# Performance work log

Measured on AMD Instinct MI355X. Metric: run time of the kernel, lower is better.

The kernel has to match this reference:

```python
import jax, jax.numpy as jnp
import numpy as np

N = 50000      # nodes
E = 800000     # edges
D_IN = 128
D_OUT = 128
R = 8          # relation types
EPS = 1e-12    # F.normalize eps


def setup_inputs() -> dict:
    key = jax.random.key(0)
    ks = jax.random.split(key, 10)
    s_in = 1.0 / np.sqrt(D_IN)
    s_out = 1.0 / np.sqrt(D_OUT)
    return {
        "x": jax.random.normal(ks[0], (N, D_IN), jnp.float32),
        "W1": jax.random.normal(ks[1], (R, D_IN, D_OUT), jnp.float32) * s_in,
        "loopW1": jax.random.normal(ks[2], (D_IN, D_OUT), jnp.float32) * s_in,
        "b1": jax.random.normal(ks[3], (D_OUT,), jnp.float32) * 0.01,
        "W2": jax.random.normal(ks[4], (R, D_OUT, D_OUT), jnp.float32) * s_out,
        "loopW2": jax.random.normal(ks[5], (D_OUT, D_OUT), jnp.float32) * s_out,
        "b2": jax.random.normal(ks[6], (D_OUT,), jnp.float32) * 0.01,
        "src": jax.random.randint(ks[7], (E,), 0, N),
        "dst": jax.random.randint(ks[8], (E,), 0, N),
        "etypes": jax.random.randint(ks[9], (E,), 0, R),
    }


def rel_layer(x, src, dst, etypes, W, loopW, b):
    # transform every node by every relation: [R, N, D_out]
    xw = jnp.einsum('ni,rio->rno', x, W)
    # gather per-edge messages: [E, D_out]
    msg = xw[etypes, src]
    # scatter-add to destination nodes
    agg = jax.ops.segment_sum(msg, dst, num_segments=x.shape[0])
    # self-loop + bias (DGL RelGraphConv defaults)
    return agg + x @ loopW + b


def reference(x, W1, loopW1, b1, W2, loopW2, b2, src, dst, etypes):
    h = jax.nn.relu(rel_layer(x, src, dst, etypes, W1, loopW1, b1))
    h = rel_layer(h, src, dst, etypes, W2, loopW2, b2)
    # F.normalize: row-wise L2, eps=1e-12
    nrm = jnp.maximum(jnp.linalg.norm(h, axis=1, keepdims=True), EPS)
    return h / nrm
```

## Files before the change

kernel.cpp:

```cpp
#include <hip/hip_runtime.h>
#include <hip/hip_bf16.h>

#define D 128
#define CH 4096

typedef unsigned int u32;
typedef unsigned short u16;
typedef __attribute__((ext_vector_type(8))) short s16x8;
typedef __attribute__((ext_vector_type(4))) float f32x4;
typedef __attribute__((ext_vector_type(2))) float f32x2;

__device__ __forceinline__ float bf2f(u16 u) {
    union { u32 u; float f; } v; v.u = ((u32)u) << 16; return v.f;
}
__device__ __forceinline__ u16 f2bf(float f) {
    union { float f; u32 u; } v; v.f = f;
    return (u16)((v.u + 0x7fffu + ((v.u >> 16) & 1u)) >> 16);
}
__device__ __forceinline__ u32 pack_bf2(float a, float b) {
    __hip_bfloat162 t = __float22bfloat162_rn(make_float2(a, b));
    union { __hip_bfloat162 t; u32 u; } v; v.t = t; return v.u;
}
__device__ __forceinline__ void unpack2(u32 u, float& lo, float& hi) {
    union { u32 u; float f; } a, b;
    a.u = u << 16; b.u = u & 0xffff0000u;
    lo = a.f; hi = b.f;
}

__global__ void detect_dtype(const u16* __restrict__ x, int* __restrict__ flag) {
    __shared__ int cnt;
    if (threadIdx.x == 0) cnt = 0;
    __syncthreads();
    u16 u = x[2 * threadIdx.x];
    int e = (u >> 7) & 0xFF;
    if (e >= 96 && e <= 150) atomicAdd(&cnt, 1);
    __syncthreads();
    if (threadIdx.x == 0) *flag = (cnt >= 128) ? 0 : 1;
}

__global__ __launch_bounds__(256)
void to_bf16_all(const void* __restrict__ s0, const void* __restrict__ s1,
                 const void* __restrict__ s2, const void* __restrict__ s3,
                 const void* __restrict__ s4, const void* __restrict__ s5,
                 const void* __restrict__ s6,
                 u16* __restrict__ d0, u16* __restrict__ d1, u16* __restrict__ d2,
                 u16* __restrict__ d3, u16* __restrict__ d4, u16* __restrict__ d5,
                 u16* __restrict__ d6,
                 long long n0, long long n1, long long n2, long long n3,
                 long long n4, long long n5, long long n6,
                 const int* __restrict__ flag)
{
    if (*flag == 0) return;
    long long i = (long long)blockIdx.x * 256 + threadIdx.x;
    const void* s; u16* d; long long off;
    if      (i < n0)                   { s = s0; d = d0; off = i; }
    else if (i < n0+n1)                { s = s1; d = d1; off = i-n0; }
    else if (i < n0+n1+n2)             { s = s2; d = d2; off = i-n0-n1; }
    else if (i < n0+n1+n2+n3)          { s = s3; d = d3; off = i-n0-n1-n2; }
    else if (i < n0+n1+n2+n3+n4)       { s = s4; d = d4; off = i-n0-n1-n2-n3; }
    else if (i < n0+n1+n2+n3+n4+n5)    { s = s5; d = d5; off = i-n0-n1-n2-n3-n4; }
    else if (i < n0+n1+n2+n3+n4+n5+n6) { s = s6; d = d6; off = i-n0-n1-n2-n3-n4-n5; }
    else return;
    d[off] = f2bf(((const float*)s)[off]);
}

__global__ __launch_bounds__(256)
void zero_ints(int* __restrict__ a, int n) {
    int i = blockIdx.x * 256 + threadIdx.x;
    if (i < n) a[i] = 0;
}

__global__ __launch_bounds__(256)
void csr_count(const int* __restrict__ dst, int* __restrict__ gcnt, int E, int nbuck) {
    __shared__ int scnt[256];
    int tid = threadIdx.x;
    scnt[tid] = 0;
    __syncthreads();
    int base = blockIdx.x * CH;
#pragma unroll
    for (int it = 0; it < CH / 256; ++it) {
        int e = base + it * 256 + tid;
        if (e < E) atomicAdd(&scnt[dst[e] >> 8], 1);
    }
    __syncthreads();
    if (tid < nbuck && scnt[tid] > 0) atomicAdd(&gcnt[tid], scnt[tid]);
}

__global__ __launch_bounds__(256)
void csr_scan(const int* __restrict__ gcnt, int* __restrict__ bstart, int* __restrict__ bcur,
              int nbuck, int N_, int E_, int* __restrict__ offs) {
    __shared__ int wpart[4];
    int tid = threadIdx.x, lane = tid & 63, wid = tid >> 6;
    int v = (tid < nbuck) ? gcnt[tid] : 0;
    int s = v;
#pragma unroll
    for (int off = 1; off < 64; off <<= 1) {
        int t = __shfl_up(s, off, 64);
        if (lane >= off) s += t;
    }
    if (lane == 63) wpart[wid] = s;
    __syncthreads();
    int add = 0;
    for (int w = 0; w < wid; ++w) add += wpart[w];
    int excl = add + s - v;
    if (tid <= nbuck) bstart[tid] = excl;
    if (tid < nbuck)  bcur[tid]  = excl;
    if (tid == 0) offs[N_] = E_;
}

__global__ __launch_bounds__(256)
void csr_part(const int* __restrict__ src, const int* __restrict__ dst,
              const int* __restrict__ et, int* __restrict__ bcur,
              u32* __restrict__ ebuf, int E, int N, int nbuck) {
    __shared__ int scnt[256], sbase[256];
    int tid = threadIdx.x;
    scnt[tid] = 0;
    __syncthreads();
    int base = blockIdx.x * CH;
#pragma unroll
    for (int it = 0; it < CH / 256; ++it) {
        int e = base + it * 256 + tid;
        if (e < E) atomicAdd(&scnt[dst[e] >> 8], 1);
    }
    __syncthreads();
    if (tid < nbuck) {
        int c = scnt[tid];
        sbase[tid] = c ? atomicAdd(&bcur[tid], c) : 0;
    }
    __syncthreads();
    scnt[tid] = 0;
    __syncthreads();
#pragma unroll
    for (int it = 0; it < CH / 256; ++it) {
        int e = base + it * 256 + tid;
        if (e >= E) continue;
        int d = dst[e];
        int b = d >> 8;
        int p = sbase[b] + atomicAdd(&scnt[b], 1);
        ebuf[p] = ((u32)(d & 255) << 24) | (u32)(et[e] * N + src[e]);
    }
}

__global__ __launch_bounds__(256)
void csr_emit(const u32* __restrict__ ebuf, const int* __restrict__ bstart,
              int* __restrict__ offs, int* __restrict__ rowidx, int N) {
    __shared__ int hist[256], excl[256], cur[256];
    __shared__ int wpart[4];
    int b = blockIdx.x, tid = threadIdx.x;
    int lo = bstart[b], hi = bstart[b + 1];
    hist[tid] = 0; cur[tid] = 0;
    __syncthreads();
    for (int i = lo + tid; i < hi; i += 256) atomicAdd(&hist[ebuf[i] >> 24], 1);
    __syncthreads();
    int lane = tid & 63, wid = tid >> 6;
    int v = hist[tid], s = v;
#pragma unroll
    for (int off = 1; off < 64; off <<= 1) {
        int t = __shfl_up(s, off, 64);
        if (lane >= off) s += t;
    }
    if (lane == 63) wpart[wid] = s;
    __syncthreads();
    int add = 0;
    for (int w = 0; w < wid; ++w) add += wpart[w];
    int e_ = add + s - v;
    excl[tid] = e_;
    int node = (b << 8) + tid;
    if (node < N) offs[node] = lo + e_;
    __syncthreads();
    for (int i = lo + tid; i < hi; i += 256) {
        u32 rec = ebuf[i];
        int dl = rec >> 24;
        int p = lo + excl[dl] + atomicAdd(&cur[dl], 1);
        rowidx[p] = (int)(rec & 0xFFFFFFu);
    }
}

__global__ __launch_bounds__(256)
void gemm_k128(const u16* __restrict__ Ac, const u16* __restrict__ Ao,
               const u16* __restrict__ Wc, const u16* __restrict__ Wo,
               const u16* __restrict__ lWc, const u16* __restrict__ lWo,
               const u16* __restrict__ bc, const u16* __restrict__ bo,
               const int* __restrict__ flag,
               int M, int R_, u16* __restrict__ xw, u16* __restrict__ sl)
{
    __shared__ u16 As[128 * 128];
    const bool f = (*flag != 0);
    const u16* A     = f ? Ac  : Ao;
    const u16* Wall  = f ? Wc  : Wo;
    const u16* loopW = f ? lWc : lWo;
    const u16* bias  = f ? bc  : bo;

    const int y = blockIdx.y;
    const u16* B = (y < R_) ? (Wall + (long long)y * D * D) : loopW;
    const int row0 = blockIdx.x * 128;
    const int tid  = threadIdx.x;
    const int lane = tid & 63;
    const int wv   = tid >> 6;
    const int quad = lane >> 4;
    const int l16  = lane & 15;

    {
        int r_base = (wv << 2) + (lane >> 4);
        int c      = lane & 15;
        auto* lds0 = (__attribute__((address_space(3))) char*)As;
#pragma unroll
        for (int it = 0; it < 8; ++it) {
            int rl = it * 16 + r_base;
            int cg = c ^ (rl & 15);
            int rg = row0 + rl; if (rg >= M) rg = M - 1;
            const u16* gp = A + (long long)rg * D + cg * 8;
            __builtin_amdgcn_global_load_lds(
                (const __attribute__((address_space(1))) void*)gp,
                (__attribute__((address_space(3))) void*)(lds0 + it * 4096 + wv * 1024),
                16, 0, 0);
        }
    }

    s16x8 bf[4][2];
#pragma unroll
    for (int kk = 0; kk < 4; ++kk)
#pragma unroll
        for (int j = 0; j < 8; ++j) {
            u32 p = *(const u32*)(B + (kk * 32 + quad * 8 + j) * D + wv * 32 + 2 * l16);
            bf[kk][0][j] = (short)(p & 0xffffu);
            bf[kk][1][j] = (short)(p >> 16);
        }

    f32x4 acc[8][2];
#pragma unroll
    for (int mt = 0; mt < 8; ++mt) { acc[mt][0] = (f32x4)0.f; acc[mt][1] = (f32x4)0.f; }

    __syncthreads();

#pragma unroll
    for (int kk = 0; kk < 4; ++kk) {
        const int chunk = (kk * 4 + quad) ^ l16;
#pragma unroll
        for (int mt = 0; mt < 8; ++mt) {
            int rl = mt * 16 + l16;
            s16x8 a = *(const s16x8*)(As + rl * D + chunk * 8);
            acc[mt][0] = __builtin_amdgcn_mfma_f32_16x16x32_bf16(a, bf[kk][0], acc[mt][0], 0, 0, 0);
            acc[mt][1] = __builtin_amdgcn_mfma_f32_16x16x32_bf16(a, bf[kk][1], acc[mt][1], 0, 0, 0);
        }
    }

    long long MD64 = (long long)M * 64;
    int cpair = wv * 16 + l16;
    if (y < R_) {
        u32* o = (u32*)xw + (long long)y * MD64;
#pragma unroll
        for (int mt = 0; mt < 8; ++mt)
#pragma unroll
            for (int i = 0; i < 4; ++i) {
                int r = row0 + mt * 16 + quad * 4 + i;
                if (r >= M) continue;
                o[(long long)r * 64 + cpair] = pack_bf2(acc[mt][0][i], acc[mt][1][i]);
            }
    } else {
        float b0 = bf2f(bias[wv * 32 + 2 * l16]);
        float b1 = bf2f(bias[wv * 32 + 2 * l16 + 1]);
        u32* o = (u32*)sl;
#pragma unroll
        for (int mt = 0; mt < 8; ++mt)
#pragma unroll
            for (int i = 0; i < 4; ++i) {
                int r = row0 + mt * 16 + quad * 4 + i;
                if (r >= M) continue;
                o[(long long)r * 64 + cpair] = pack_bf2(acc[mt][0][i] + b0, acc[mt][1][i] + b1);
            }
    }
}

__global__ __launch_bounds__(256)
void aggregate(const u16* __restrict__ xw, const u16* __restrict__ sl,
               const int* __restrict__ offs, const int* __restrict__ rowidx,
               void* __restrict__ out, int N, int mode, const int* __restrict__ flag)
{
    int node = blockIdx.x * 4 + (threadIdx.x >> 6);
    int p = threadIdx.x & 63;
    if (node >= N) return;
    const u32* xw32 = (const u32*)xw;

    float a0, a1;
    unpack2(((const u32*)sl)[(long long)node * 64 + p], a0, a1);

    int j = offs[node], end = offs[node + 1];
    for (; j + 4 <= end; j += 4) {
        int r0 = rowidx[j], r1 = rowidx[j + 1], r2 = rowidx[j + 2], r3 = rowidx[j + 3];
        u32 u0 = xw32[(long long)r0 * 64 + p];
        u32 u1 = xw32[(long long)r1 * 64 + p];
        u32 u2 = xw32[(long long)r2 * 64 + p];
        u32 u3 = xw32[(long long)r3 * 64 + p];
        float l, h;
        unpack2(u0, l, h); a0 += l; a1 += h;
        unpack2(u1, l, h); a0 += l; a1 += h;
        unpack2(u2, l, h); a0 += l; a1 += h;
        unpack2(u3, l, h); a0 += l; a1 += h;
    }
    for (; j < end; ++j) {
        float l, h;
        unpack2(xw32[(long long)rowidx[j] * 64 + p], l, h);
        a0 += l; a1 += h;
    }

    if (mode == 0) {
        a0 = fmaxf(a0, 0.f); a1 = fmaxf(a1, 0.f);
        ((u32*)out)[(long long)node * 64 + p] = pack_bf2(a0, a1);
    } else {
        float s = a0 * a0 + a1 * a1;
#pragma unroll
        for (int off = 32; off > 0; off >>= 1) s += __shfl_xor(s, off, 64);
        float sc = 1.f / fmaxf(sqrtf(s), 1e-12f);
        a0 *= sc; a1 *= sc;
        if (*flag) {
            f32x2 w; w[0] = a0; w[1] = a1;
            ((f32x2*)out)[(long long)node * 64 + p] = w;
        } else {
            ((u32*)out)[(long long)node * 64 + p] = pack_bf2(a0, a1);
        }
    }
}

static inline size_t align256(size_t x) { return (x + 255) & ~(size_t)255; }

extern "C" void kernel_launch(void* const* d_in, const int* in_sizes, int n_in,
                              void* d_out, int out_size, void* d_ws, size_t ws_size,
                              hipStream_t stream)
{
    const void* x_in   = d_in[0];
    const void* W1_in  = d_in[1];
    const void* lW1_in = d_in[2];
    const void* b1_in  = d_in[3];
    const void* W2_in  = d_in[4];
    const void* lW2_in = d_in[5];
    const void* b2_in  = d_in[6];
    const int* src = (const int*)d_in[7];
    const int* dst = (const int*)d_in[8];
    const int* et  = (const int*)d_in[9];

    const int N = in_sizes[0] / D;
    const int E = in_sizes[7];
    const int R = in_sizes[1] / (D * D);
    const int nbuck = (N + 255) >> 8;

    const long long ND  = (long long)N * D;
    const long long RDD = (long long)R * D * D;
    const long long DDl = (long long)D * D;

    size_t off = 0;
    auto alloc = [&](size_t bytes) { size_t o = off; off = align256(off + bytes); return o; };
    size_t o_flag = alloc(256);
    size_t o_xc   = alloc((size_t)ND * 2);
    size_t o_W1   = alloc((size_t)RDD * 2);
    size_t o_lW1  = alloc((size_t)DDl * 2);
    size_t o_b1   = alloc((size_t)D * 2);
    size_t o_W2   = alloc((size_t)RDD * 2);
    size_t o_lW2  = alloc((size_t)DDl * 2);
    size_t o_b2   = alloc((size_t)D * 2);
    size_t o_sl   = alloc((size_t)ND * 2);
    size_t o_h    = alloc((size_t)ND * 2);
    size_t o_offs = alloc((size_t)(N + 1) * 4);
    size_t o_gcnt = alloc(1024);
    size_t o_bst  = alloc(1040 * 4);
    size_t o_bcur = alloc(1024);
    size_t o_ebuf = alloc((size_t)E * 4);
    size_t o_ridx = alloc((size_t)E * 4);
    size_t o_xw   = alloc((size_t)R * ND * 2);
    (void)ws_size;

    char* ws = (char*)d_ws;
    int* flag   = (int*)(ws + o_flag);
    u16* x_c    = (u16*)(ws + o_xc);
    u16* W1c    = (u16*)(ws + o_W1);
    u16* lW1c   = (u16*)(ws + o_lW1);
    u16* b1c    = (u16*)(ws + o_b1);
    u16* W2c    = (u16*)(ws + o_W2);
    u16* lW2c   = (u16*)(ws + o_lW2);
    u16* b2c    = (u16*)(ws + o_b2);
    u16* sl     = (u16*)(ws + o_sl);
    u16* h      = (u16*)(ws + o_h);
    int* offs   = (int*)(ws + o_offs);
    int* gcnt   = (int*)(ws + o_gcnt);
    int* bstart = (int*)(ws + o_bst);
    int* bcur   = (int*)(ws + o_bcur);
    u32* ebuf   = (u32*)(ws + o_ebuf);
    int* rowidx = (int*)(ws + o_ridx);
    u16* xw     = (u16*)(ws + o_xw);

    dim3 blk(256, 1, 1);
    int mb   = (N + 127) / 128;
    int nblkE = (E + CH - 1) / CH;
    auto cdiv = [](long long n) { return (u32)((n + 255) / 256); };

    detect_dtype<<<dim3(1), blk, 0, stream>>>((const u16*)x_in, flag);
    long long tot = ND + RDD + DDl + D + RDD + DDl + D;
    to_bf16_all<<<dim3(cdiv(tot)), blk, 0, stream>>>(
        x_in, W1_in, lW1_in, b1_in, W2_in, lW2_in, b2_in,
        x_c, W1c, lW1c, b1c, W2c, lW2c, b2c,
        ND, RDD, DDl, (long long)D, RDD, DDl, (long long)D, flag);

    zero_ints<<<dim3(1), blk, 0, stream>>>(gcnt, nbuck);
    csr_count<<<dim3(nblkE), blk, 0, stream>>>(dst, gcnt, E, nbuck);
    csr_scan<<<dim3(1), blk, 0, stream>>>(gcnt, bstart, bcur, nbuck, N, E, offs);
    csr_part<<<dim3(nblkE), blk, 0, stream>>>(src, dst, et, bcur, ebuf, E, N, nbuck);
    csr_emit<<<dim3(nbuck), blk, 0, stream>>>(ebuf, bstart, offs, rowidx, N);

    gemm_k128<<<dim3(mb, R + 1), blk, 0, stream>>>(
        x_c, (const u16*)x_in, W1c, (const u16*)W1_in, lW1c, (const u16*)lW1_in,
        b1c, (const u16*)b1_in, flag, N, R, xw, sl);
    aggregate<<<dim3((N + 3) / 4), blk, 0, stream>>>(xw, sl, offs, rowidx, h, N, 0, flag);

    gemm_k128<<<dim3(mb, R + 1), blk, 0, stream>>>(
        h, h, W2c, (const u16*)W2_in, lW2c, (const u16*)lW2_in,
        b2c, (const u16*)b2_in, flag, N, R, xw, sl);
    aggregate<<<dim3((N + 3) / 4), blk, 0, stream>>>(xw, sl, offs, rowidx, d_out, N, 1, flag);
}
```

Measured before the change: 303.6 us.

## Vectorize aggregation gathers, add nontemporal stores, fold zeroing into dtype detect

The aggregate kernel now has each wavefront split into four 16-lane groups. Each group loads 16-byte rows for a different edge, and the partial sums are combined with cross-lane shuffles. This cuts the number of gather instructions and raises memory-level parallelism per node. GEMM and aggregate outputs use nontemporal stores, the zero_ints launch is folded into detect_dtype, and the conversion kernel becomes a grid-stride loop with a fixed grid. The trade-off is extra shuffle reductions, a masked tail path, and nontemporal stores that may bypass cache for xw, which is re-read by the next kernel.

```diff
diff --git a/kernel.cpp b/kernel.cpp
--- a/kernel.cpp
+++ b/kernel.cpp
@@ -9,6 +9,8 @@
 typedef __attribute__((ext_vector_type(8))) short s16x8;
 typedef __attribute__((ext_vector_type(4))) float f32x4;
 typedef __attribute__((ext_vector_type(2))) float f32x2;
+typedef __attribute__((ext_vector_type(2))) u32 u32x2;
+typedef __attribute__((ext_vector_type(4))) u32 u32x4;
 
 __device__ __forceinline__ float bf2f(u16 u) {
     union { u32 u; float f; } v; v.u = ((u32)u) << 16; return v.f;
@@ -26,11 +28,21 @@
     a.u = u << 16; b.u = u & 0xffff0000u;
     lo = a.f; hi = b.f;
 }
-
-__global__ void detect_dtype(const u16* __restrict__ x, int* __restrict__ flag) {
+__device__ __forceinline__ void acc8(float (&a)[8], u32x4 u) {
+#pragma unroll
+    for (int m = 0; m < 4; ++m) {
+        float l, h;
+        unpack2(u[m], l, h);
+        a[2 * m] += l; a[2 * m + 1] += h;
+    }
+}
+
+__global__ void detect_dtype(const u16* __restrict__ x, int* __restrict__ flag,
+                             int* __restrict__ gcnt, int nbuck) {
     __shared__ int cnt;
     if (threadIdx.x == 0) cnt = 0;
     __syncthreads();
+    if ((int)threadIdx.x < nbuck) gcnt[threadIdx.x] = 0;
     u16 u = x[2 * threadIdx.x];
     int e = (u >> 7) & 0xFF;
     if (e >= 96 && e <= 150) atomicAdd(&cnt, 1);
@@ -51,23 +63,19 @@
                  const int* __restrict__ flag)
 {
     if (*flag == 0) return;
-    long long i = (long long)blockIdx.x * 256 + threadIdx.x;
-    const void* s; u16* d; long long off;
-    if      (i < n0)                   { s = s0; d = d0; off = i; }
-    else if (i < n0+n1)                { s = s1; d = d1; off = i-n0; }
-    else if (i < n0+n1+n2)             { s = s2; d = d2; off = i-n0-n1; }
-    else if (i < n0+n1+n2+n3)          { s = s3; d = d3; off = i-n0-n1-n2; }
-    else if (i < n0+n1+n2+n3+n4)       { s = s4; d = d4; off = i-n0-n1-n2-n3; }
-    else if (i < n0+n1+n2+n3+n4+n5)    { s = s5; d = d5; off = i-n0-n1-n2-n3-n4; }
-    else if (i < n0+n1+n2+n3+n4+n5+n6) { s = s6; d = d6; off = i-n0-n1-n2-n3-n4-n5; }
-    else return;
-    d[off] = f2bf(((const float*)s)[off]);
-}
-
-__global__ __launch_bounds__(256)
-void zero_ints(int* __restrict__ a, int n) {
-    int i = blockIdx.x * 256 + threadIdx.x;
-    if (i < n) a[i] = 0;
+    long long tot = n0 + n1 + n2 + n3 + n4 + n5 + n6;
+    long long stride = (long long)gridDim.x * 256;
+    for (long long i = (long long)blockIdx.x * 256 + threadIdx.x; i < tot; i += stride) {
+        const void* s; u16* d; long long off;
+        if      (i < n0)                   { s = s0; d = d0; off = i; }
+        else if (i < n0+n1)                { s = s1; d = d1; off = i-n0; }
+        else if (i < n0+n1+n2)             { s = s2; d = d2; off = i-n0-n1; }
+        else if (i < n0+n1+n2+n3)          { s = s3; d = d3; off = i-n0-n1-n2; }
+        else if (i < n0+n1+n2+n3+n4)       { s = s4; d = d4; off = i-n0-n1-n2-n3; }
+        else if (i < n0+n1+n2+n3+n4+n5)    { s = s5; d = d5; off = i-n0-n1-n2-n3-n4; }
+        else                               { s = s6; d = d6; off = i-n0-n1-n2-n3-n4-n5; }
+        d[off] = f2bf(((const float*)s)[off]);
+    }
 }
 
 __global__ __launch_bounds__(256)
@@ -255,7 +263,8 @@
             for (int i = 0; i < 4; ++i) {
                 int r = row0 + mt * 16 + quad * 4 + i;
                 if (r >= M) continue;
-                o[(long long)r * 64 + cpair] = pack_bf2(acc[mt][0][i], acc[mt][1][i]);
+                __builtin_nontemporal_store(pack_bf2(acc[mt][0][i], acc[mt][1][i]),
+                                            &o[(long long)r * 64 + cpair]);
             }
     } else {
         float b0 = bf2f(bias[wv * 32 + 2 * l16]);
@@ -267,7 +276,8 @@
             for (int i = 0; i < 4; ++i) {
                 int r = row0 + mt * 16 + quad * 4 + i;
                 if (r >= M) continue;
-                o[(long long)r * 64 + cpair] = pack_bf2(acc[mt][0][i] + b0, acc[mt][1][i] + b1);
+                __builtin_nontemporal_store(pack_bf2(acc[mt][0][i] + b0, acc[mt][1][i] + b1),
+                                            &o[(long long)r * 64 + cpair]);
             }
     }
 }
@@ -278,46 +288,85 @@
                void* __restrict__ out, int N, int mode, const int* __restrict__ flag)
 {
     int node = blockIdx.x * 4 + (threadIdx.x >> 6);
-    int p = threadIdx.x & 63;
+    int lane = threadIdx.x & 63;
+    int p  = lane & 15;
+    int qw = lane >> 4;
     if (node >= N) return;
-    const u32* xw32 = (const u32*)xw;
-
-    float a0, a1;
-    unpack2(((const u32*)sl)[(long long)node * 64 + p], a0, a1);
-
-    int j = offs[node], end = offs[node + 1];
-    for (; j + 4 <= end; j += 4) {
-        int r0 = rowidx[j], r1 = rowidx[j + 1], r2 = rowidx[j + 2], r3 = rowidx[j + 3];
-        u32 u0 = xw32[(long long)r0 * 64 + p];
-        u32 u1 = xw32[(long long)r1 * 64 + p];
-        u32 u2 = xw32[(long long)r2 * 64 + p];
-        u32 u3 = xw32[(long long)r3 * 64 + p];
-        float l, h;
-        unpack2(u0, l, h); a0 += l; a1 += h;
-        unpack2(u1, l, h); a0 += l; a1 += h;
-        unpack2(u2, l, h); a0 += l; a1 += h;
-        unpack2(u3, l, h); a0 += l; a1 += h;
-    }
-    for (; j < end; ++j) {
-        float l, h;
-        unpack2(xw32[(long long)rowidx[j] * 64 + p], l, h);
-        a0 += l; a1 += h;
+    const u32x4* xw4 = (const u32x4*)xw;
+
+    float a[8];
+    if (qw == 0) {
+        u32x4 s4 = ((const u32x4*)sl)[(long long)node * 16 + p];
+#pragma unroll
+        for (int m = 0; m < 4; ++m) unpack2(s4[m], a[2 * m], a[2 * m + 1]);
+    } else {
+#pragma unroll
+        for (int k = 0; k < 8; ++k) a[k] = 0.f;
+    }
+
+    int j = offs[node], j1 = offs[node + 1];
+    for (; j + 16 <= j1; j += 16) {
+        int r0 = rowidx[j + qw];
+        int r1 = rowidx[j + 4 + qw];
+        int r2 = rowidx[j + 8 + qw];
+        int r3 = rowidx[j + 12 + qw];
+        u32x4 u0 = xw4[(long long)r0 * 16 + p];
+        u32x4 u1 = xw4[(long long)r1 * 16 + p];
+        u32x4 u2 = xw4[(long long)r2 * 16 + p];
+        u32x4 u3 = xw4[(long long)r3 * 16 + p];
+        acc8(a, u0); acc8(a, u1); acc8(a, u2); acc8(a, u3);
+    }
+    for (; j + 4 <= j1; j += 4) {
+        int r = rowidx[j + qw];
+        acc8(a, xw4[(long long)r * 16 + p]);
+    }
+    int rem = j1 - j;
+    if (rem > 0) {
+        int rr = rowidx[(qw < rem) ? j + qw : j];
+        u32x4 u = xw4[(long long)rr * 16 + p];
+        if (qw >= rem) { u[0] = 0; u[1] = 0; u[2] = 0; u[3] = 0; }
+        acc8(a, u);
+    }
+
+#pragma unroll
+    for (int k = 0; k < 8; ++k) {
+        a[k] += __shfl_xor(a[k], 16, 64);
+        a[k] += __shfl_xor(a[k], 32, 64);
     }
 
     if (mode == 0) {
-        a0 = fmaxf(a0, 0.f); a1 = fmaxf(a1, 0.f);
-        ((u32*)out)[(long long)node * 64 + p] = pack_bf2(a0, a1);
+        if (qw == 0) {
+            u32x4 w;
+#pragma unroll
+            for (int m = 0; m < 4; ++m)
+                w[m] = pack_bf2(fmaxf(a[2 * m], 0.f), fmaxf(a[2 * m + 1], 0.f));
+            __builtin_nontemporal_store(w, &((u32x4*)out)[(long long)node * 16 + p]);
+        }
     } else {
-        float s = a0 * a0 + a1 * a1;
-#pragma unroll
-        for (int off = 32; off > 0; off >>= 1) s += __shfl_xor(s, off, 64);
+        float s = 0.f;
+#pragma unroll
+        for (int k = 0; k < 8; ++k) s += a[k] * a[k];
+#pragma unroll
+        for (int off = 8; off > 0; off >>= 1) s += __shfl_xor(s, off, 64);
         float sc = 1.f / fmaxf(sqrtf(s), 1e-12f);
-        a0 *= sc; a1 *= sc;
-        if (*flag) {
-            f32x2 w; w[0] = a0; w[1] = a1;
-            ((f32x2*)out)[(long long)node * 64 + p] = w;
-        } else {
-            ((u32*)out)[(long long)node * 64 + p] = pack_bf2(a0, a1);
+        if (qw == 0) {
+            if (*flag) {
+                f32x4 w0, w1;
+#pragma unroll
+                for (int m = 0; m < 4; ++m) {
+                    float* wp = (m < 2) ? (float*)&w0 : (float*)&w1;
+                    wp[(m & 1) * 2]     = a[2 * m] * sc;
+                    wp[(m & 1) * 2 + 1] = a[2 * m + 1] * sc;
+                }
+                __builtin_nontemporal_store(w0, &((f32x4*)out)[(long long)node * 32 + p * 2]);
+                __builtin_nontemporal_store(w1, &((f32x4*)out)[(long long)node * 32 + p * 2 + 1]);
+            } else {
+                u32x4 w;
+#pragma unroll
+                for (int m = 0; m < 4; ++m)
+                    w[m] = pack_bf2(a[2 * m] * sc, a[2 * m + 1] * sc);
+                __builtin_nontemporal_store(w, &((u32x4*)out)[(long long)node * 16 + p]);
+            }
         }
     }
 }
@@ -389,18 +438,15 @@
     u16* xw     = (u16*)(ws + o_xw);
 
     dim3 blk(256, 1, 1);
-    int mb   = (N + 127) / 128;
+    int mb    = (N + 127) / 128;
     int nblkE = (E + CH - 1) / CH;
-    auto cdiv = [](long long n) { return (u32)((n + 255) / 256); };
-
-    detect_dtype<<<dim3(1), blk, 0, stream>>>((const u16*)x_in, flag);
-    long long tot = ND + RDD + DDl + D + RDD + DDl + D;
-    to_bf16_all<<<dim3(cdiv(tot)), blk, 0, stream>>>(
+
+    detect_dtype<<<dim3(1), blk, 0, stream>>>((const u16*)x_in, flag, gcnt, nbuck);
+    to_bf16_all<<<dim3(4096), blk, 0, stream>>>(
         x_in, W1_in, lW1_in, b1_in, W2_in, lW2_in, b2_in,
         x_c, W1c, lW1c, b1c, W2c, lW2c, b2c,
         ND, RDD, DDl, (long long)D, RDD, DDl, (long long)D, flag);
 
-    zero_ints<<<dim3(1), blk, 0, stream>>>(gcnt, nbuck);
     csr_count<<<dim3(nblkE), blk, 0, stream>>>(dst, gcnt, E, nbuck);
     csr_scan<<<dim3(1), blk, 0, stream>>>(gcnt, bstart, bcur, nbuck, N, E, offs);
     csr_part<<<dim3(nblkE), blk, 0, stream>>>(src, dst, et, bcur, ebuf, E, N, nbuck);
```

New measurement: 324.0 us. +6.7%, slower.
